# Performance work log

Hardware: AMD Instinct MI355X
Metric: run time of the kernel (lower is better)

Reference implementation:

```python
import itertools
import jax, jax.numpy as jnp
import numpy as np

ALPHA = 1e-4   # mse/conn mixing
BETA = 0.1
DMAX = 20.0
NCAP = 10.0    # costs_n_cap
PCAP = 3.0     # costs_p_cap
W3D = 64       # 3D cube window (window_3d)
W2D = 32       # 2D MALIS window (window_2d, default)


def _dilate5(mask):
    # scipy binary_dilation, default cross structuring element, 5 iterations
    m = mask.astype(bool)
    for _ in range(5):
        p = np.pad(m, 1)
        m = p[1:-1, 1:-1] | p[:-2, 1:-1] | p[2:, 1:-1] | p[1:-1, :-2] | p[1:-1, 2:]
    return m


def _label8(mask):
    # skimage.measure.label on boolean mask: 8-connectivity, background=0
    H, W = mask.shape
    lbl = np.zeros((H, W), np.int64)
    parent = {}

    def find(x):
        while parent[x] != x:
            parent[x] = parent[parent[x]]
            x = parent[x]
        return x

    nxt = 1
    for i in range(H):
        for j in range(W):
            if not mask[i, j]:
                continue
            neigh = []
            for di, dj in ((-1, -1), (-1, 0), (-1, 1), (0, -1)):
                ii, jj = i + di, j + dj
                if 0 <= ii < H and 0 <= jj < W and mask[ii, jj]:
                    neigh.append(int(lbl[ii, jj]))
            if not neigh:
                lbl[i, j] = nxt
                parent[nxt] = nxt
                nxt += 1
            else:
                m0 = min(neigh)
                lbl[i, j] = m0
                for nb in neigh:
                    ra, rb = find(m0), find(nb)
                    if ra != rb:
                        parent[max(ra, rb)] = min(ra, rb)
    out = np.zeros_like(lbl)
    remap = {}
    c = 0
    for i in range(H):
        for j in range(W):
            if lbl[i, j] > 0:
                r = find(int(lbl[i, j]))
                if r not in remap:
                    c += 1
                    remap[r] = c
                out[i, j] = remap[r]
    return out


def _malis_edge_weights(seg, n1, n2, costs, pos):
    # MALIS union-find / Kruskal maximal-spanning-tree pair counting.
    # Edges processed in descending cost order. Background (seg==0) nodes
    # are not counted. pos=1: #same-label pairs merged; pos=0: #diff-label pairs.
    n = seg.size
    parent = list(range(n))

    def find(x):
        r = x
        while parent[r] != r:
            r = parent[r]
        while parent[x] != r:
            parent[x], x = r, parent[x]
        return r

    cnt = [({int(s): 1} if s > 0 else {}) for s in seg]
    tot = [1 if s > 0 else 0 for s in seg]
    w = np.zeros(costs.shape[0], np.float32)
    for e in np.argsort(-costs, kind="stable"):
        ra, rb = find(int(n1[e])), find(int(n2[e]))
        if ra == rb:
            continue
        ca, cb = cnt[ra], cnt[rb]
        if len(ca) > len(cb):
            ra, rb, ca, cb = rb, ra, cb, ca
        same = 0
        for l, v in ca.items():
            same += v * cb.get(l, 0)
        w[e] = float(same if pos else tot[ra] * tot[rb] - same)
        for l, v in ca.items():
            cb[l] = cb.get(l, 0) + v
        tot[rb] += tot[ra]
        parent[ra] = rb
        cnt[ra] = None
    return w


def _window_weights(pred2d, tgt2d):
    # numpy MALIS node weights for a [B,1,H,W] 2D projection
    B, C, H, W = pred2d.shape
    w = W2D
    wn = np.zeros(pred2d.shape, np.float32)
    wp = np.zeros(pred2d.shape, np.float32)
    idx = np.arange(w * w).reshape(w, w)
    n1 = np.concatenate([idx[:, :-1].ravel(), idx[:-1, :].ravel()])
    n2 = np.concatenate([idx[:, 1:].ravel(), idx[1:, :].ravel()])
    nh = w * (w - 1)
    for k in range(H // w):
        for j in range(W // w):
            p = pred2d[:, :, k*w:(k+1)*w, j*w:(j+1)*w]
            t = tgt2d[:, :, k*w:(k+1)*w, j*w:(j+1)*w]
            ch = (p[:, :, :, :-1] + p[:, :, :, 1:]).reshape(B, -1)
            cv = (p[:, :, :-1, :] + p[:, :, 1:, :]).reshape(B, -1)
            costs = np.concatenate([ch, cv], 1).astype(np.float32)
            gh = (t[:, :, :, :-1] + t[:, :, :, 1:]).reshape(B, -1)
            gv = (t[:, :, :-1, :] + t[:, :, 1:, :]).reshape(B, -1)
            gt = np.concatenate([gh, gv], 1).astype(np.float32)
            costs_n = costs.copy()
            costs_p = costs.copy()
            costs_n[gt > NCAP] = NCAP
            costs_p[gt < PCAP] = 0.0
            gt = np.minimum(gt, NCAP)
            for b in range(B):
                sg = _label8(~_dilate5(t[b, 0] == 0)).ravel()
                en = _malis_edge_weights(sg, n1, n2, costs_n[b], 0)
                ep = _malis_edge_weights(sg, n1, n2, costs_p[b], 1)
                sn = en.sum()
                if sn > 0:
                    en = en / sn
                sp = ep.sum()
                if sp > 0:
                    ep = ep / sp
                en[gt[b] >= PCAP] = 0.0
                ep[gt[b] < NCAP] = 0.0
                for ew, out in ((en, wn), (ep, wp)):
                    eh = ew[:nh].reshape(w, w - 1)
                    ev = ew[nh:].reshape(w - 1, w)
                    nwt = np.zeros((w, w), np.float32)
                    nwt[:, :-1] += eh
                    nwt[:, 1:] += eh
                    nwt[:-1, :] += ev
                    nwt[1:, :] += ev
                    out[b, 0, k*w:(k+1)*w, j*w:(j+1)*w] = nwt
    return wn, wp


def _precompute(pred_np, tgt_np):
    # host-side (detached) MALIS weight maps, exactly as the torch module
    B, C, H, W, D = pred_np.shape
    items = []
    for k, j, i in itertools.product(range(H // W3D), range(W // W3D), range(D // W3D)):
        sl = (slice(None), slice(None), slice(k*W3D, (k+1)*W3D),
              slice(j*W3D, (j+1)*W3D), slice(i*W3D, (i+1)*W3D))
        pc, tc = pred_np[sl], tgt_np[sl]
        for axis in (2, 3, 4):
            wn, wp = _window_weights(pc.min(axis=axis), tc.min(axis=axis))
            items.append((k, j, i, axis, jnp.asarray(wn), jnp.asarray(wp)))
    return items


def _loss(pred, target, items):
    mse = jnp.mean((pred - target) ** 2)
    conn = jnp.float32(0.0)
    for (k, j, i, axis, wn, wp) in items:
        pc = pred[:, :, k*W3D:(k+1)*W3D, j*W3D:(j+1)*W3D, i*W3D:(i+1)*W3D]
        proj = jnp.min(pc, axis=axis)  # [B,1,64,64]
        conn = conn + jnp.sum(proj**2 * wn + BETA * (DMAX - proj)**2 * wp)
    return (mse, jnp.float32(ALPHA) * conn)


def setup_inputs() -> dict:
    # synthetic distance-transform-like volumes (zeros on 'vessel' seeds)
    rng = np.random.default_rng(0)
    B, H = 4, 128
    g = np.arange(H, dtype=np.float32)
    zz, yy, xx = np.meshgrid(g, g, g, indexing="ij")
    tgt = np.empty((B, 1, H, H, H), np.float32)
    for b in range(B):
        pts = rng.uniform(0, H, size=(24, 3)).astype(np.float32)
        d = np.full((H, H, H), np.inf, np.float32)
        for p in pts:
            d = np.minimum(d, np.sqrt((zz - p[0])**2 + (yy - p[1])**2 + (xx - p[2])**2))
        tgt[b, 0] = np.floor(np.minimum(d, DMAX))
    pred = np.clip(tgt + 0.5 * rng.standard_normal(tgt.shape).astype(np.float32), 0.0, DMAX).astype(np.float32)
    return {"pred": jnp.asarray(pred), "target": jnp.asarray(tgt)}


def reference(pred, target):
    items = _precompute(np.asarray(pred), np.asarray(target))
    return _loss(pred, target, items)
```

## Files before the change

kernel.cpp:

```cpp
#include <hip/hip_runtime.h>

#define BLOCK 256
#define NNODE 1024
#define NH    992
#define NE    1984
#define NSORT 2048
#define LMAX  12
#define CHUNK 64
#define NPASS (NE / CHUNK)

typedef unsigned long long ull;

__device__ __forceinline__ void edge_nodes(int e, int& a, int& b) {
    if (e < NH) {
        int r = e / 31;
        int c = e - r * 31;
        a = (r << 5) + c;
        b = a + 1;
    } else {
        a = e - NH;
        b = a + 32;
    }
}

__device__ __forceinline__ int find_par(unsigned short* par, int x) {
    volatile unsigned short* vp = par;
    int r = x;
    int p = vp[r];
    while (p != r) { r = p; p = vp[r]; }
    int c = x;
    while (c != r) { const int nxt = vp[c]; vp[c] = (unsigned short)r; c = nxt; }
    return r;
}

__device__ __forceinline__ int dot16x4(ull a, ull b) {
    int s  = (int)(a & 0xFFFFu)         * (int)(b & 0xFFFFu);
    s     += (int)((a >> 16) & 0xFFFFu) * (int)((b >> 16) & 0xFFFFu);
    s     += (int)((a >> 32) & 0xFFFFu) * (int)((b >> 32) & 0xFFFFu);
    s     += (int)((a >> 48) & 0xFFFFu) * (int)((b >> 48) & 0xFFFFu);
    return s;
}

__device__ __forceinline__ void cswap(unsigned int& ka, unsigned short& ia,
                                      unsigned int& kb, unsigned short& ib, bool up) {
    const bool gt = (ka > kb) || (ka == kb && ia > ib);
    if (gt == up) {
        const unsigned int  tk = ka; ka = kb; kb = tk;
        const unsigned short ti = ia; ia = ib; ib = ti;
    }
}

template<int MODE>
__device__ __forceinline__ void kruskal_run(unsigned short* sh_parent,
                                            unsigned int*   sh_szto,
                                            ull*            sh_cnt64,
                                            unsigned int*   sh_key,
                                            const unsigned short* sh_idx,
                                            const int sign, const int lane) {
    unsigned int* claim32 = (unsigned int*)sh_cnt64;
    for (int pass = 0; pass < NPASS; ++pass) {
        const int e = sh_idx[pass * CHUNK + lane];
        int a, bb; edge_nodes(e, a, bb);
        int ra = find_par(sh_parent, a);
        int rb = find_par(sh_parent, bb);
        bool cand = (ra != rb);

        if (MODE < 3) {
            for (int round = 0; round < 3; ++round) {
                const unsigned int tag =
                    ((unsigned int)(pass * 4 + round + 1) << 6) | (unsigned int)(63 - lane);
                const int ia = ra * 6 + 2 * MODE;
                const int ib = rb * 6 + 2 * MODE;
                if (cand) {
                    atomicMax(&claim32[ia], tag);
                    atomicMax(&claim32[ib], tag);
                }
                asm volatile("s_waitcnt lgkmcnt(0)" ::: "memory");
                __builtin_amdgcn_sched_barrier(0);
                bool win = false;
                if (cand) win = (claim32[ia] == tag) && (claim32[ib] == tag);
                if (win) {
                    const unsigned int xa = sh_szto[ra], xb = sh_szto[rb];
                    const int ta = (int)(xa >> 16), tb = (int)(xb >> 16);
                    int wv;
                    ull a0 = 0, a1 = 0, b0 = 0, b1 = 0;
                    if (MODE == 0) {
                        wv = ta * tb;
                    } else {
                        a0 = sh_cnt64[ra * 3]; b0 = sh_cnt64[rb * 3];
                        int same = dot16x4(a0, b0);
                        if (MODE >= 2) {
                            a1 = sh_cnt64[ra * 3 + 1]; b1 = sh_cnt64[rb * 3 + 1];
                            same += dot16x4(a1, b1);
                        }
                        wv = sign ? same : (ta * tb - same);
                    }
                    const int big = ((xa & 0xFFFFu) > (xb & 0xFFFFu));
                    const int rs = big ? ra : rb;
                    const int rl = big ? rb : ra;
                    sh_key[e] = __float_as_uint((float)wv);
                    sh_szto[rs] = xa + xb;
                    if (MODE >= 1 && (ta + tb) > 0) {
                        sh_cnt64[rs * 3] = a0 + b0;
                        if (MODE >= 2) sh_cnt64[rs * 3 + 1] = a1 + b1;
                    }
                    sh_parent[rl] = (unsigned short)rs;
                    cand = false;
                }
                asm volatile("s_waitcnt lgkmcnt(0)" ::: "memory");
                __builtin_amdgcn_sched_barrier(0);
                if (cand) {
                    ra = find_par(sh_parent, ra);
                    rb = find_par(sh_parent, rb);
                    cand = (ra != rb);
                }
                const ull P = __ballot(cand);
                if (__popcll(P) < 10) break;
            }
        }

        ull m = __ballot(cand);
        while (m) {
            const int i = (int)__builtin_ctzll(m);
            m &= m - 1;
            const unsigned int pack = (unsigned int)ra | ((unsigned int)rb << 10) | ((unsigned int)e << 20);
            const unsigned int pk = (unsigned int)__shfl((int)pack, i);
            const int ra_i = (int)(pk & 1023u);
            const int rb_i = (int)((pk >> 10) & 1023u);
            if (ra_i == rb_i) continue;
            const int se = (int)(pk >> 20);
            const unsigned int xa = sh_szto[ra_i], xb = sh_szto[rb_i];
            const int ta = (int)(xa >> 16), tb = (int)(xb >> 16);
            const int big = ((xa & 0xFFFFu) > (xb & 0xFFFFu));
            const int rs = big ? ra_i : rb_i;
            const int rl = big ? rb_i : ra_i;
            int wv;
            if (MODE == 0) {
                wv = ta * tb;
            } else {
                const ull a0 = sh_cnt64[ra_i * 3 + 0];
                const ull b0 = sh_cnt64[rb_i * 3 + 0];
                ull a1 = 0, a2 = 0, b1 = 0, b2 = 0;
                int same = dot16x4(a0, b0);
                if (MODE >= 2) {
                    a1 = sh_cnt64[ra_i * 3 + 1]; b1 = sh_cnt64[rb_i * 3 + 1];
                    same += dot16x4(a1, b1);
                }
                if (MODE >= 3) {
                    a2 = sh_cnt64[ra_i * 3 + 2]; b2 = sh_cnt64[rb_i * 3 + 2];
                    same += dot16x4(a2, b2);
                }
                wv = sign ? same : (ta * tb - same);
                if (lane == 0 && (ta + tb) > 0) {
                    sh_cnt64[rs * 3 + 0] = a0 + b0;
                    if (MODE >= 2) sh_cnt64[rs * 3 + 1] = a1 + b1;
                    if (MODE >= 3) sh_cnt64[rs * 3 + 2] = a2 + b2;
                }
            }
            if (lane == 0) {
                sh_key[se] = __float_as_uint((float)wv);
                sh_szto[rs] = xa + xb;
                sh_parent[rl] = (unsigned short)rs;
            }
            if (ra == rl) ra = rs;
            if (rb == rl) rb = rs;
        }
    }
}

template<int MODE>
__device__ __forceinline__ void uf_init(unsigned short* sh_parent,
                                        unsigned int* sh_szto,
                                        ull* sh_cnt64,
                                        const unsigned char* sh_seg,
                                        const int tid) {
    for (int pix = tid; pix < NNODE; pix += BLOCK) {
        sh_parent[pix] = (unsigned short)pix;
        const int s = sh_seg[pix];
        const unsigned int tot = (s > 0 && s <= LMAX) ? 1u : 0u;
        sh_szto[pix] = 1u | (tot << 16);
        ull c0 = 0, c1 = 0, c2 = 0;
        if (s >= 1 && s <= LMAX) {
            const ull bit = 1ull << (((s - 1) & 3) * 16);
            const int q = (s - 1) >> 2;
            if (q == 0) c0 = bit; else if (q == 1) c1 = bit; else c2 = bit;
        }
        if (MODE == 0) {
            sh_cnt64[pix * 3 + 0] = 0ull;
        } else if (MODE == 1) {
            sh_cnt64[pix * 3 + 0] = c0;
            sh_cnt64[pix * 3 + 1] = 0ull;
        } else if (MODE == 2) {
            sh_cnt64[pix * 3 + 0] = c0;
            sh_cnt64[pix * 3 + 1] = c1;
            sh_cnt64[pix * 3 + 2] = 0ull;
        } else {
            sh_cnt64[pix * 3 + 0] = c0;
            sh_cnt64[pix * 3 + 1] = c1;
            sh_cnt64[pix * 3 + 2] = c2;
        }
    }
}

__global__ __launch_bounds__(BLOCK) void prep_kernel(const float* __restrict__ pred,
                                                     const float* __restrict__ tgt,
                                                     char* __restrict__ ws,
                                                     double* __restrict__ acc_ws,
                                                     int B) {
    __shared__ alignas(16) float sh_p[NNODE];
    __shared__ alignas(16) float sh_t[NNODE];
    __shared__ unsigned char  mA[NNODE];
    __shared__ unsigned char  mB[NNODE];
    __shared__ unsigned short sh_parent[NNODE];
    __shared__ unsigned short sh_lab[NNODE];
    __shared__ int sh_flag;
    __shared__ int sh_L;
    __shared__ double sh_redp[4];

    const int tid = threadIdx.x;
    const int w = blockIdx.x;
    int wg = w;
    const int b    = wg % B;  wg /= B;
    const int win  = wg & 3;  wg >>= 2;
    const int item = wg;
    const int axis_id = item % 3;
    const int cube = item / 3;
    const int ci = cube & 1;
    const int cj = (cube >> 1) & 1;
    const int ck = (cube >> 2) & 1;
    const int wk = win >> 1;
    const int wj = win & 1;

    const int NW = 96 * B;
    float* Pb = (float*)(ws + 64);
    float* Tb = Pb + (size_t)NW * NNODE;
    unsigned char* Sb = (unsigned char*)(Tb + (size_t)NW * NNODE);
    int* Lb = (int*)(Sb + (size_t)NW * NNODE);

    const size_t base = (size_t)b * 2097152u;

    if (axis_id == 2) {
        double msum = 0.0;
        for (int pix = tid; pix < NNODE; pix += BLOCK) {
            const int r = pix >> 5, c = pix & 31;
            const int R = wk * 32 + r, C = wj * 32 + c;
            const size_t idx0 = base + (size_t)(ck * 64 + R) * 16384u + (size_t)(cj * 64 + C) * 128u + (size_t)(ci * 64);
            const float4* pp = reinterpret_cast<const float4*>(pred + idx0);
            const float4* tp = reinterpret_cast<const float4*>(tgt + idx0);
            float pm = 3.4e38f, tm = 3.4e38f;
            #pragma unroll
            for (int h = 0; h < 16; ++h) {
                const float4 a = pp[h];
                const float4 t = tp[h];
                pm = fminf(pm, fminf(fminf(a.x, a.y), fminf(a.z, a.w)));
                tm = fminf(tm, fminf(fminf(t.x, t.y), fminf(t.z, t.w)));
                const float dx = a.x - t.x, dy = a.y - t.y;
                const float dz = a.z - t.z, dw = a.w - t.w;
                msum += (double)(dx * dx);
                msum += (double)(dy * dy);
                msum += (double)(dz * dz);
                msum += (double)(dw * dw);
            }
            sh_p[pix] = pm;
            sh_t[pix] = tm;
        }
        for (int off = 32; off > 0; off >>= 1) msum += __shfl_down(msum, off, 64);
        if ((tid & 63) == 0) sh_redp[tid >> 6] = msum;
        __syncthreads();
        if (tid == 0)
            atomicAdd(&acc_ws[0], sh_redp[0] + sh_redp[1] + sh_redp[2] + sh_redp[3]);
    } else {
        const int r  = tid >> 3;
        const int c0 = (tid & 7) << 2;
        const int R = wk * 32 + r, C = wj * 32 + c0;
        size_t idx0; int hstride;
        if (axis_id == 0) {
            idx0 = base + (size_t)(ck * 64) * 16384u + (size_t)(cj * 64 + R) * 128u + (size_t)(ci * 64 + C);
            hstride = 16384;
        } else {
            idx0 = base + (size_t)(ck * 64 + R) * 16384u + (size_t)(cj * 64) * 128u + (size_t)(ci * 64 + C);
            hstride = 128;
        }
        float4 pm = make_float4(3.4e38f, 3.4e38f, 3.4e38f, 3.4e38f);
        float4 tm = pm;
        #pragma unroll 8
        for (int h = 0; h < 64; ++h) {
            const float4 a  = *reinterpret_cast<const float4*>(pred + idx0);
            const float4 t4 = *reinterpret_cast<const float4*>(tgt + idx0);
            pm.x = fminf(pm.x, a.x);  pm.y = fminf(pm.y, a.y);
            pm.z = fminf(pm.z, a.z);  pm.w = fminf(pm.w, a.w);
            tm.x = fminf(tm.x, t4.x); tm.y = fminf(tm.y, t4.y);
            tm.z = fminf(tm.z, t4.z); tm.w = fminf(tm.w, t4.w);
            idx0 += (size_t)hstride;
        }
        *reinterpret_cast<float4*>(&sh_p[(r << 5) + c0]) = pm;
        *reinterpret_cast<float4*>(&sh_t[(r << 5) + c0]) = tm;
        __syncthreads();
    }

    for (int pix = tid; pix < NNODE; pix += BLOCK)
        mA[pix] = (sh_t[pix] == 0.0f) ? 1 : 0;
    __syncthreads();
    for (int it = 0; it < 5; ++it) {
        unsigned char* src = (it & 1) ? mB : mA;
        unsigned char* dst = (it & 1) ? mA : mB;
        for (int pix = tid; pix < NNODE; pix += BLOCK) {
            const int r = pix >> 5, c = pix & 31;
            unsigned char v = src[pix];
            if (r > 0)  v |= src[pix - 32];
            if (r < 31) v |= src[pix + 32];
            if (c > 0)  v |= src[pix - 1];
            if (c < 31) v |= src[pix + 1];
            dst[pix] = v;
        }
        __syncthreads();
    }
    for (int pix = tid; pix < NNODE; pix += BLOCK)
        mA[pix] = mB[pix] ^ 1;
    __syncthreads();

    for (int pix = tid; pix < NNODE; pix += BLOCK)
        sh_parent[pix] = mA[pix] ? (unsigned short)pix : (unsigned short)0xFFFF;
    __syncthreads();
    for (;;) {
        if (tid == 0) sh_flag = 0;
        __syncthreads();
        for (int pix = tid; pix < NNODE; pix += BLOCK) {
            if (!mA[pix]) continue;
            const int r = pix >> 5, c = pix & 31;
            int m = sh_parent[pix];
            #pragma unroll
            for (int d = 0; d < 8; ++d) {
                static const int dr[8] = {-1,-1,-1, 0, 0, 1, 1, 1};
                static const int dc[8] = {-1, 0, 1,-1, 1,-1, 0, 1};
                const int rr = r + dr[d], cc = c + dc[d];
                if (rr < 0 || rr > 31 || cc < 0 || cc > 31) continue;
                const int nb = (rr << 5) + cc;
                if (mA[nb]) { int v = sh_parent[nb]; if (v < m) m = v; }
            }
            while ((int)sh_parent[m] < m) m = sh_parent[m];
            if (m < (int)sh_parent[pix]) { sh_parent[pix] = (unsigned short)m; sh_flag = 1; }
        }
        __syncthreads();
        const int f = sh_flag;
        __syncthreads();
        if (f == 0) break;
    }

    if (tid == 0) sh_L = 0;
    __syncthreads();
    for (int pix = tid; pix < NNODE; pix += BLOCK) {
        if (mA[pix] && (int)sh_parent[pix] == pix) {
            const int id = atomicAdd(&sh_L, 1);
            sh_lab[pix] = (unsigned short)(id + 1);
        }
    }
    __syncthreads();

    {
        const int p4 = tid << 2;
        *reinterpret_cast<float4*>(&Pb[(size_t)w * NNODE + p4]) =
            *reinterpret_cast<const float4*>(&sh_p[p4]);
        *reinterpret_cast<float4*>(&Tb[(size_t)w * NNODE + p4]) =
            *reinterpret_cast<const float4*>(&sh_t[p4]);
        unsigned int packed = 0;
        #pragma unroll
        for (int q = 0; q < 4; ++q) {
            const int pix = p4 + q;
            unsigned int s = 0;
            if (mA[pix]) {
                int lab = sh_lab[sh_parent[pix]];
                if (lab > 255) lab = 255;
                s = (unsigned int)lab;
            }
            packed |= s << (q * 8);
        }
        ((unsigned int*)Sb)[(size_t)w * (NNODE / 4) + tid] = packed;
        if (tid == 0) Lb[w] = sh_L;
    }
}

__global__ __launch_bounds__(BLOCK) void solve_kernel(const char* __restrict__ ws_c,
                                                      double* __restrict__ acc_ws,
                                                      int B) {
    __shared__ alignas(16) float          sh_p[NNODE];
    __shared__ alignas(16) float          sh_t[NNODE];
    __shared__ alignas(16) unsigned int   sh_key[NSORT];
    __shared__ alignas(16) unsigned short sh_idx[NSORT];
    __shared__ unsigned short sh_parent[NNODE];
    __shared__ unsigned int   sh_szto[NNODE];
    __shared__ ull            sh_cnt64[NNODE * 3];
    __shared__ alignas(16) unsigned char sh_seg[NNODE];
    __shared__ float          sh_sn;
    __shared__ double         sh_red[4];

    const int tid = threadIdx.x;
    int wg = blockIdx.x;
    const int sign = wg & 1;  wg >>= 1;
    const int w = wg;

    const int NW = 96 * B;
    const float* Pb = (const float*)(ws_c + 64);
    const float* Tb = Pb + (size_t)NW * NNODE;
    const unsigned char* Sb = (const unsigned char*)(Tb + (size_t)NW * NNODE);
    const int* Lb = (const int*)(Sb + (size_t)NW * NNODE);

    const int Lraw = Lb[w];
    if (Lraw == 0 || (Lraw == 1 && sign == 0)) return;
    const int mode = (Lraw <= 1) ? 0 : ((Lraw <= 4) ? 1 : ((Lraw <= 8) ? 2 : 3));

    {
        const int p4 = tid << 2;
        *reinterpret_cast<float4*>(&sh_p[p4]) =
            *reinterpret_cast<const float4*>(&Pb[(size_t)w * NNODE + p4]);
        *reinterpret_cast<float4*>(&sh_t[p4]) =
            *reinterpret_cast<const float4*>(&Tb[(size_t)w * NNODE + p4]);
        ((unsigned int*)sh_seg)[tid] =
            ((const unsigned int*)Sb)[(size_t)w * (NNODE / 4) + tid];
    }
    __syncthreads();

    if (mode == 0)      uf_init<0>(sh_parent, sh_szto, sh_cnt64, sh_seg, tid);
    else if (mode == 1) uf_init<1>(sh_parent, sh_szto, sh_cnt64, sh_seg, tid);
    else if (mode == 2) uf_init<2>(sh_parent, sh_szto, sh_cnt64, sh_seg, tid);
    else                uf_init<3>(sh_parent, sh_szto, sh_cnt64, sh_seg, tid);
    __syncthreads();

    unsigned int   K[8];
    unsigned short I[8];
    const int b8 = tid << 3;
    #pragma unroll
    for (int l = 0; l < 8; ++l) {
        const int e = b8 + l;
        if (e < NE) {
            int a, bb; edge_nodes(e, a, bb);
            float cost = sh_p[a] + sh_p[bb];
            const float g = sh_t[a] + sh_t[bb];
            if (sign == 0) { if (g > 10.0f) cost = 10.0f; }
            else           { if (g <  3.0f) cost = 0.0f;  }
            K[l] = ~__float_as_uint(cost);
            I[l] = (unsigned short)e;
        } else {
            K[l] = 0xFFFFFFFFu;
            I[l] = (unsigned short)0xFFFF;
        }
    }
    cswap(K[0],I[0],K[1],I[1], true );
    cswap(K[2],I[2],K[3],I[3], false);
    cswap(K[4],I[4],K[5],I[5], true );
    cswap(K[6],I[6],K[7],I[7], false);
    cswap(K[0],I[0],K[2],I[2], true );
    cswap(K[1],I[1],K[3],I[3], true );
    cswap(K[4],I[4],K[6],I[6], false);
    cswap(K[5],I[5],K[7],I[7], false);
    cswap(K[0],I[0],K[1],I[1], true );
    cswap(K[2],I[2],K[3],I[3], true );
    cswap(K[4],I[4],K[5],I[5], false);
    cswap(K[6],I[6],K[7],I[7], false);
    {
        const bool u8 = ((b8 & 8) == 0);
        cswap(K[0],I[0],K[4],I[4], u8); cswap(K[1],I[1],K[5],I[5], u8);
        cswap(K[2],I[2],K[6],I[6], u8); cswap(K[3],I[3],K[7],I[7], u8);
        cswap(K[0],I[0],K[2],I[2], u8); cswap(K[1],I[1],K[3],I[3], u8);
        cswap(K[4],I[4],K[6],I[6], u8); cswap(K[5],I[5],K[7],I[7], u8);
        cswap(K[0],I[0],K[1],I[1], u8); cswap(K[2],I[2],K[3],I[3], u8);
        cswap(K[4],I[4],K[5],I[5], u8); cswap(K[6],I[6],K[7],I[7], u8);
    }
    {
        uint4 k0, k1, iv;
        k0.x=K[0]; k0.y=K[1]; k0.z=K[2]; k0.w=K[3];
        k1.x=K[4]; k1.y=K[5]; k1.z=K[6]; k1.w=K[7];
        iv.x=(unsigned int)I[0] | ((unsigned int)I[1]<<16);
        iv.y=(unsigned int)I[2] | ((unsigned int)I[3]<<16);
        iv.z=(unsigned int)I[4] | ((unsigned int)I[5]<<16);
        iv.w=(unsigned int)I[6] | ((unsigned int)I[7]<<16);
        *reinterpret_cast<uint4*>(&sh_key[b8])     = k0;
        *reinterpret_cast<uint4*>(&sh_key[b8 + 4]) = k1;
        *reinterpret_cast<uint4*>(&sh_idx[b8])     = iv;
    }
    __syncthreads();

    for (int k = 16; k <= NSORT; k <<= 1) {
        for (int j = k >> 1; j >= 8; j >>= 1) {
            for (int p = tid; p < (NSORT >> 1); p += BLOCK) {
                const int i   = ((p & ~(j - 1)) << 1) | (p & (j - 1));
                const int ixj = i | j;
                const unsigned int ka = sh_key[i], kb = sh_key[ixj];
                const unsigned short ia = sh_idx[i], ib = sh_idx[ixj];
                const bool gt = (ka > kb) || (ka == kb && ia > ib);
                const bool up = ((i & k) == 0);
                if (gt == up) {
                    sh_key[i] = kb; sh_key[ixj] = ka;
                    sh_idx[i] = ib; sh_idx[ixj] = ia;
                }
            }
            __syncthreads();
        }
        {
            const uint4 k0 = *reinterpret_cast<const uint4*>(&sh_key[b8]);
            const uint4 k1 = *reinterpret_cast<const uint4*>(&sh_key[b8 + 4]);
            const uint4 iv = *reinterpret_cast<const uint4*>(&sh_idx[b8]);
            K[0]=k0.x; K[1]=k0.y; K[2]=k0.z; K[3]=k0.w;
            K[4]=k1.x; K[5]=k1.y; K[6]=k1.z; K[7]=k1.w;
            I[0]=(unsigned short)(iv.x); I[1]=(unsigned short)(iv.x>>16);
            I[2]=(unsigned short)(iv.y); I[3]=(unsigned short)(iv.y>>16);
            I[4]=(unsigned short)(iv.z); I[5]=(unsigned short)(iv.z>>16);
            I[6]=(unsigned short)(iv.w); I[7]=(unsigned short)(iv.w>>16);
            const bool u8 = ((b8 & k) == 0);
            cswap(K[0],I[0],K[4],I[4], u8); cswap(K[1],I[1],K[5],I[5], u8);
            cswap(K[2],I[2],K[6],I[6], u8); cswap(K[3],I[3],K[7],I[7], u8);
            cswap(K[0],I[0],K[2],I[2], u8); cswap(K[1],I[1],K[3],I[3], u8);
            cswap(K[4],I[4],K[6],I[6], u8); cswap(K[5],I[5],K[7],I[7], u8);
            cswap(K[0],I[0],K[1],I[1], u8); cswap(K[2],I[2],K[3],I[3], u8);
            cswap(K[4],I[4],K[5],I[5], u8); cswap(K[6],I[6],K[7],I[7], u8);
            uint4 o0, o1, ov;
            o0.x=K[0]; o0.y=K[1]; o0.z=K[2]; o0.w=K[3];
            o1.x=K[4]; o1.y=K[5]; o1.z=K[6]; o1.w=K[7];
            ov.x=(unsigned int)I[0] | ((unsigned int)I[1]<<16);
            ov.y=(unsigned int)I[2] | ((unsigned int)I[3]<<16);
            ov.z=(unsigned int)I[4] | ((unsigned int)I[5]<<16);
            ov.w=(unsigned int)I[6] | ((unsigned int)I[7]<<16);
            *reinterpret_cast<uint4*>(&sh_key[b8])     = o0;
            *reinterpret_cast<uint4*>(&sh_key[b8 + 4]) = o1;
            *reinterpret_cast<uint4*>(&sh_idx[b8])     = ov;
        }
        __syncthreads();
    }

    for (int e = tid; e < NE; e += BLOCK) sh_key[e] = 0u;
    __syncthreads();

    if (tid < 64) {
        if (mode == 0)      kruskal_run<0>(sh_parent, sh_szto, sh_cnt64, sh_key, sh_idx, sign, tid);
        else if (mode == 1) kruskal_run<1>(sh_parent, sh_szto, sh_cnt64, sh_key, sh_idx, sign, tid);
        else if (mode == 2) kruskal_run<2>(sh_parent, sh_szto, sh_cnt64, sh_key, sh_idx, sign, tid);
        else                kruskal_run<3>(sh_parent, sh_szto, sh_cnt64, sh_key, sh_idx, sign, tid);
    }
    __syncthreads();

    {
        float part = 0.0f;
        for (int e = tid; e < NE; e += BLOCK) part += __uint_as_float(sh_key[e]);
        for (int off = 32; off > 0; off >>= 1) part += __shfl_down(part, off, 64);
        if ((tid & 63) == 0) sh_red[tid >> 6] = (double)part;
        __syncthreads();
        if (tid == 0) sh_sn = (float)(sh_red[0] + sh_red[1] + sh_red[2] + sh_red[3]);
        __syncthreads();
    }
    const float sn = sh_sn;

    double acc = 0.0;
    for (int pix = tid; pix < NNODE; pix += BLOCK) {
        const int r = pix >> 5, c = pix & 31;
        float nw = 0.0f;
        if (c < 31) { const int e = r * 31 + c;
            float v = __uint_as_float(sh_key[e]); if (sn > 0.0f) v = v / sn;
            const float g = sh_t[pix] + sh_t[pix + 1];
            if (sign == 0) { if (g >= 3.0f) v = 0.0f; } else { if (g < 10.0f) v = 0.0f; }
            nw += v; }
        if (c > 0)  { const int e = r * 31 + c - 1;
            float v = __uint_as_float(sh_key[e]); if (sn > 0.0f) v = v / sn;
            const float g = sh_t[pix - 1] + sh_t[pix];
            if (sign == 0) { if (g >= 3.0f) v = 0.0f; } else { if (g < 10.0f) v = 0.0f; }
            nw += v; }
        if (r < 31) { const int e = NH + pix;
            float v = __uint_as_float(sh_key[e]); if (sn > 0.0f) v = v / sn;
            const float g = sh_t[pix] + sh_t[pix + 32];
            if (sign == 0) { if (g >= 3.0f) v = 0.0f; } else { if (g < 10.0f) v = 0.0f; }
            nw += v; }
        if (r > 0)  { const int e = NH + pix - 32;
            float v = __uint_as_float(sh_key[e]); if (sn > 0.0f) v = v / sn;
            const float g = sh_t[pix - 32] + sh_t[pix];
            if (sign == 0) { if (g >= 3.0f) v = 0.0f; } else { if (g < 10.0f) v = 0.0f; }
            nw += v; }
        const float p = sh_p[pix];
        float term;
        if (sign == 0) term = (p * p) * nw;
        else { const float d = 20.0f - p; term = (0.1f * (d * d)) * nw; }
        acc += (double)term;
    }
    for (int off = 32; off > 0; off >>= 1) acc += __shfl_down(acc, off, 64);
    if ((tid & 63) == 0) sh_red[tid >> 6] = acc;
    __syncthreads();
    if (tid == 0)
        atomicAdd(&acc_ws[1], sh_red[0] + sh_red[1] + sh_red[2] + sh_red[3]);
}

__global__ __launch_bounds__(BLOCK) void conn_kernel(const float* __restrict__ pred,
                                                     const float* __restrict__ tgt,
                                                     double* __restrict__ acc_ws,
                                                     int B) {
    __shared__ alignas(16) float          sh_p[NNODE];
    __shared__ alignas(16) float          sh_t[NNODE];
    __shared__ alignas(16) unsigned int   sh_key[NSORT];
    __shared__ alignas(16) unsigned short sh_idx[NSORT];
    __shared__ unsigned short sh_parent[NNODE];
    __shared__ unsigned int   sh_szto[NNODE];
    __shared__ ull            sh_cnt64[NNODE * 3];
    __shared__ unsigned char  sh_seg[NNODE];
    __shared__ int            sh_flag;
    __shared__ int            sh_L;
    __shared__ float          sh_sn;
    __shared__ double         sh_red[4];

    const int tid = threadIdx.x;
    int wg = blockIdx.x;
    const int sign = (wg >> 3) & 1;
    wg = (wg & 7) | ((wg >> 4) << 3);
    const int b    = wg % B;  wg /= B;
    const int win  = wg & 3;  wg >>= 2;
    const int item = wg;
    const int axis_id = item % 3;
    const int cube = item / 3;
    const int ci = cube & 1;
    const int cj = (cube >> 1) & 1;
    const int ck = (cube >> 2) & 1;
    const int wk = win >> 1;
    const int wj = win & 1;

    const size_t base = (size_t)b * 2097152u;

    if (axis_id == 2) {
        for (int pix = tid; pix < NNODE; pix += BLOCK) {
            const int r = pix >> 5, c = pix & 31;
            const int R = wk * 32 + r, C = wj * 32 + c;
            const size_t idx0 = base + (size_t)(ck * 64 + R) * 16384u + (size_t)(cj * 64 + C) * 128u + (size_t)(ci * 64);
            const float4* pp = reinterpret_cast<const float4*>(pred + idx0);
            const float4* tp = reinterpret_cast<const float4*>(tgt + idx0);
            float pm = 3.4e38f, tm = 3.4e38f;
            #pragma unroll
            for (int h = 0; h < 16; ++h) {
                const float4 a = pp[h];
                const float4 t = tp[h];
                pm = fminf(pm, fminf(fminf(a.x, a.y), fminf(a.z, a.w)));
                tm = fminf(tm, fminf(fminf(t.x, t.y), fminf(t.z, t.w)));
            }
            sh_p[pix] = pm;
            sh_t[pix] = tm;
        }
    } else {
        const int r  = tid >> 3;
        const int c0 = (tid & 7) << 2;
        const int R = wk * 32 + r, C = wj * 32 + c0;
        size_t idx0; int hstride;
        if (axis_id == 0) {
            idx0 = base + (size_t)(ck * 64) * 16384u + (size_t)(cj * 64 + R) * 128u + (size_t)(ci * 64 + C);
            hstride = 16384;
        } else {
            idx0 = base + (size_t)(ck * 64 + R) * 16384u + (size_t)(cj * 64) * 128u + (size_t)(ci * 64 + C);
            hstride = 128;
        }
        float4 pm = make_float4(3.4e38f, 3.4e38f, 3.4e38f, 3.4e38f);
        float4 tm = pm;
        #pragma unroll 8
        for (int h = 0; h < 64; ++h) {
            const float4 a  = *reinterpret_cast<const float4*>(pred + idx0);
            const float4 t4 = *reinterpret_cast<const float4*>(tgt + idx0);
            pm.x = fminf(pm.x, a.x);  pm.y = fminf(pm.y, a.y);
            pm.z = fminf(pm.z, a.z);  pm.w = fminf(pm.w, a.w);
            tm.x = fminf(tm.x, t4.x); tm.y = fminf(tm.y, t4.y);
            tm.z = fminf(tm.z, t4.z); tm.w = fminf(tm.w, t4.w);
            idx0 += (size_t)hstride;
        }
        *reinterpret_cast<float4*>(&sh_p[(r << 5) + c0]) = pm;
        *reinterpret_cast<float4*>(&sh_t[(r << 5) + c0]) = tm;
    }
    __syncthreads();

    unsigned char* mA = sh_seg;
    unsigned char* mB = (unsigned char*)sh_idx;
    for (int pix = tid; pix < NNODE; pix += BLOCK)
        mA[pix] = (sh_t[pix] == 0.0f) ? 1 : 0;
    __syncthreads();
    for (int it = 0; it < 5; ++it) {
        unsigned char* src = (it & 1) ? mB : mA;
        unsigned char* dst = (it & 1) ? mA : mB;
        for (int pix = tid; pix < NNODE; pix += BLOCK) {
            const int r = pix >> 5, c = pix & 31;
            unsigned char v = src[pix];
            if (r > 0)  v |= src[pix - 32];
            if (r < 31) v |= src[pix + 32];
            if (c > 0)  v |= src[pix - 1];
            if (c < 31) v |= src[pix + 1];
            dst[pix] = v;
        }
        __syncthreads();
    }
    for (int pix = tid; pix < NNODE; pix += BLOCK)
        mA[pix] = mB[pix] ^ 1;
    __syncthreads();

    for (int pix = tid; pix < NNODE; pix += BLOCK)
        sh_parent[pix] = mA[pix] ? (unsigned short)pix : (unsigned short)0xFFFF;
    __syncthreads();
    for (;;) {
        if (tid == 0) sh_flag = 0;
        __syncthreads();
        for (int pix = tid; pix < NNODE; pix += BLOCK) {
            if (!mA[pix]) continue;
            const int r = pix >> 5, c = pix & 31;
            int m = sh_parent[pix];
            #pragma unroll
            for (int d = 0; d < 8; ++d) {
                static const int dr[8] = {-1,-1,-1, 0, 0, 1, 1, 1};
                static const int dc[8] = {-1, 0, 1,-1, 1,-1, 0, 1};
                const int rr = r + dr[d], cc = c + dc[d];
                if (rr < 0 || rr > 31 || cc < 0 || cc > 31) continue;
                const int nb = (rr << 5) + cc;
                if (mA[nb]) { int v = sh_parent[nb]; if (v < m) m = v; }
            }
            while ((int)sh_parent[m] < m) m = sh_parent[m];
            if (m < (int)sh_parent[pix]) { sh_parent[pix] = (unsigned short)m; sh_flag = 1; }
        }
        __syncthreads();
        const int f = sh_flag;
        __syncthreads();
        if (f == 0) break;
    }

    if (tid == 0) sh_L = 0;
    __syncthreads();
    for (int pix = tid; pix < NNODE; pix += BLOCK) {
        if (mA[pix] && (int)sh_parent[pix] == pix) {
            const int id = atomicAdd(&sh_L, 1);
            sh_szto[pix] = (unsigned int)(id + 1);
        }
    }
    __syncthreads();
    for (int pix = tid; pix < NNODE; pix += BLOCK) {
        unsigned char s = 0;
        if (mA[pix]) {
            int lab = (int)sh_szto[sh_parent[pix]];
            if (lab > 255) lab = 255;
            s = (unsigned char)lab;
        }
        sh_seg[pix] = s;
    }
    __syncthreads();

    const int Lraw = sh_L;
    const int mode = (Lraw <= 1) ? 0 : ((Lraw <= 4) ? 1 : ((Lraw <= 8) ? 2 : 3));
    const bool skip_all = (Lraw == 0) || (Lraw == 1 && sign == 0);

    if (!skip_all) {

    if (mode == 0)      uf_init<0>(sh_parent, sh_szto, sh_cnt64, sh_seg, tid);
    else if (mode == 1) uf_init<1>(sh_parent, sh_szto, sh_cnt64, sh_seg, tid);
    else if (mode == 2) uf_init<2>(sh_parent, sh_szto, sh_cnt64, sh_seg, tid);
    else                uf_init<3>(sh_parent, sh_szto, sh_cnt64, sh_seg, tid);
    __syncthreads();

    unsigned int   K[8];
    unsigned short I[8];
    const int b8 = tid << 3;
    #pragma unroll
    for (int l = 0; l < 8; ++l) {
        const int e = b8 + l;
        if (e < NE) {
            int a, bb; edge_nodes(e, a, bb);
            float cost = sh_p[a] + sh_p[bb];
            const float g = sh_t[a] + sh_t[bb];
            if (sign == 0) { if (g > 10.0f) cost = 10.0f; }
            else           { if (g <  3.0f) cost = 0.0f;  }
            K[l] = ~__float_as_uint(cost);
            I[l] = (unsigned short)e;
        } else {
            K[l] = 0xFFFFFFFFu;
            I[l] = (unsigned short)0xFFFF;
        }
    }
    cswap(K[0],I[0],K[1],I[1], true );
    cswap(K[2],I[2],K[3],I[3], false);
    cswap(K[4],I[4],K[5],I[5], true );
    cswap(K[6],I[6],K[7],I[7], false);
    cswap(K[0],I[0],K[2],I[2], true );
    cswap(K[1],I[1],K[3],I[3], true );
    cswap(K[4],I[4],K[6],I[6], false);
    cswap(K[5],I[5],K[7],I[7], false);
    cswap(K[0],I[0],K[1],I[1], true );
    cswap(K[2],I[2],K[3],I[3], true );
    cswap(K[4],I[4],K[5],I[5], false);
    cswap(K[6],I[6],K[7],I[7], false);
    {
        const bool u8 = ((b8 & 8) == 0);
        cswap(K[0],I[0],K[4],I[4], u8); cswap(K[1],I[1],K[5],I[5], u8);
        cswap(K[2],I[2],K[6],I[6], u8); cswap(K[3],I[3],K[7],I[7], u8);
        cswap(K[0],I[0],K[2],I[2], u8); cswap(K[1],I[1],K[3],I[3], u8);
        cswap(K[4],I[4],K[6],I[6], u8); cswap(K[5],I[5],K[7],I[7], u8);
        cswap(K[0],I[0],K[1],I[1], u8); cswap(K[2],I[2],K[3],I[3], u8);
        cswap(K[4],I[4],K[5],I[5], u8); cswap(K[6],I[6],K[7],I[7], u8);
    }
    {
        uint4 k0, k1, iv;
        k0.x=K[0]; k0.y=K[1]; k0.z=K[2]; k0.w=K[3];
        k1.x=K[4]; k1.y=K[5]; k1.z=K[6]; k1.w=K[7];
        iv.x=(unsigned int)I[0] | ((unsigned int)I[1]<<16);
        iv.y=(unsigned int)I[2] | ((unsigned int)I[3]<<16);
        iv.z=(unsigned int)I[4] | ((unsigned int)I[5]<<16);
        iv.w=(unsigned int)I[6] | ((unsigned int)I[7]<<16);
        *reinterpret_cast<uint4*>(&sh_key[b8])     = k0;
        *reinterpret_cast<uint4*>(&sh_key[b8 + 4]) = k1;
        *reinterpret_cast<uint4*>(&sh_idx[b8])     = iv;
    }
    __syncthreads();

    for (int k = 16; k <= NSORT; k <<= 1) {
        for (int j = k >> 1; j >= 8; j >>= 1) {
            for (int p = tid; p < (NSORT >> 1); p += BLOCK) {
                const int i   = ((p & ~(j - 1)) << 1) | (p & (j - 1));
                const int ixj = i | j;
                const unsigned int ka = sh_key[i], kb = sh_key[ixj];
                const unsigned short ia = sh_idx[i], ib = sh_idx[ixj];
                const bool gt = (ka > kb) || (ka == kb && ia > ib);
                const bool up = ((i & k) == 0);
                if (gt == up) {
                    sh_key[i] = kb; sh_key[ixj] = ka;
                    sh_idx[i] = ib; sh_idx[ixj] = ia;
                }
            }
            __syncthreads();
        }
        {
            const uint4 k0 = *reinterpret_cast<const uint4*>(&sh_key[b8]);
            const uint4 k1 = *reinterpret_cast<const uint4*>(&sh_key[b8 + 4]);
            const uint4 iv = *reinterpret_cast<const uint4*>(&sh_idx[b8]);
            K[0]=k0.x; K[1]=k0.y; K[2]=k0.z; K[3]=k0.w;
            K[4]=k1.x; K[5]=k1.y; K[6]=k1.z; K[7]=k1.w;
            I[0]=(unsigned short)(iv.x); I[1]=(unsigned short)(iv.x>>16);
            I[2]=(unsigned short)(iv.y); I[3]=(unsigned short)(iv.y>>16);
            I[4]=(unsigned short)(iv.z); I[5]=(unsigned short)(iv.z>>16);
            I[6]=(unsigned short)(iv.w); I[7]=(unsigned short)(iv.w>>16);
            const bool u8 = ((b8 & k) == 0);
            cswap(K[0],I[0],K[4],I[4], u8); cswap(K[1],I[1],K[5],I[5], u8);
            cswap(K[2],I[2],K[6],I[6], u8); cswap(K[3],I[3],K[7],I[7], u8);
            cswap(K[0],I[0],K[2],I[2], u8); cswap(K[1],I[1],K[3],I[3], u8);
            cswap(K[4],I[4],K[6],I[6], u8); cswap(K[5],I[5],K[7],I[7], u8);
            cswap(K[0],I[0],K[1],I[1], u8); cswap(K[2],I[2],K[3],I[3], u8);
            cswap(K[4],I[4],K[5],I[5], u8); cswap(K[6],I[6],K[7],I[7], u8);
            uint4 o0, o1, ov;
            o0.x=K[0]; o0.y=K[1]; o0.z=K[2]; o0.w=K[3];
            o1.x=K[4]; o1.y=K[5]; o1.z=K[6]; o1.w=K[7];
            ov.x=(unsigned int)I[0] | ((unsigned int)I[1]<<16);
            ov.y=(unsigned int)I[2] | ((unsigned int)I[3]<<16);
            ov.z=(unsigned int)I[4] | ((unsigned int)I[5]<<16);
            ov.w=(unsigned int)I[6] | ((unsigned int)I[7]<<16);
            *reinterpret_cast<uint4*>(&sh_key[b8])     = o0;
            *reinterpret_cast<uint4*>(&sh_key[b8 + 4]) = o1;
            *reinterpret_cast<uint4*>(&sh_idx[b8])     = ov;
        }
        __syncthreads();
    }

    for (int e = tid; e < NE; e += BLOCK) sh_key[e] = 0u;
    __syncthreads();

    if (tid < 64) {
        if (mode == 0)      kruskal_run<0>(sh_parent, sh_szto, sh_cnt64, sh_key, sh_idx, sign, tid);
        else if (mode == 1) kruskal_run<1>(sh_parent, sh_szto, sh_cnt64, sh_key, sh_idx, sign, tid);
        else if (mode == 2) kruskal_run<2>(sh_parent, sh_szto, sh_cnt64, sh_key, sh_idx, sign, tid);
        else                kruskal_run<3>(sh_parent, sh_szto, sh_cnt64, sh_key, sh_idx, sign, tid);
    }
    __syncthreads();

    {
        float part = 0.0f;
        for (int e = tid; e < NE; e += BLOCK) part += __uint_as_float(sh_key[e]);
        for (int off = 32; off > 0; off >>= 1) part += __shfl_down(part, off, 64);
        if ((tid & 63) == 0) sh_red[tid >> 6] = (double)part;
        __syncthreads();
        if (tid == 0) sh_sn = (float)(sh_red[0] + sh_red[1] + sh_red[2] + sh_red[3]);
        __syncthreads();
    }
    const float sn = sh_sn;

    double acc = 0.0;
    for (int pix = tid; pix < NNODE; pix += BLOCK) {
        const int r = pix >> 5, c = pix & 31;
        float nw = 0.0f;
        if (c < 31) { const int e = r * 31 + c;
            float v = __uint_as_float(sh_key[e]); if (sn > 0.0f) v = v / sn;
            const float g = sh_t[pix] + sh_t[pix + 1];
            if (sign == 0) { if (g >= 3.0f) v = 0.0f; } else { if (g < 10.0f) v = 0.0f; }
            nw += v; }
        if (c > 0)  { const int e = r * 31 + c - 1;
            float v = __uint_as_float(sh_key[e]); if (sn > 0.0f) v = v / sn;
            const float g = sh_t[pix - 1] + sh_t[pix];
            if (sign == 0) { if (g >= 3.0f) v = 0.0f; } else { if (g < 10.0f) v = 0.0f; }
            nw += v; }
        if (r < 31) { const int e = NH + pix;
            float v = __uint_as_float(sh_key[e]); if (sn > 0.0f) v = v / sn;
            const float g = sh_t[pix] + sh_t[pix + 32];
            if (sign == 0) { if (g >= 3.0f) v = 0.0f; } else { if (g < 10.0f) v = 0.0f; }
            nw += v; }
        if (r > 0)  { const int e = NH + pix - 32;
            float v = __uint_as_float(sh_key[e]); if (sn > 0.0f) v = v / sn;
            const float g = sh_t[pix - 32] + sh_t[pix];
            if (sign == 0) { if (g >= 3.0f) v = 0.0f; } else { if (g < 10.0f) v = 0.0f; }
            nw += v; }
        const float p = sh_p[pix];
        float term;
        if (sign == 0) term = (p * p) * nw;
        else { const float d = 20.0f - p; term = (0.1f * (d * d)) * nw; }
        acc += (double)term;
    }
    for (int off = 32; off > 0; off >>= 1) acc += __shfl_down(acc, off, 64);
    if ((tid & 63) == 0) sh_red[tid >> 6] = acc;
    __syncthreads();
    if (tid == 0)
        atomicAdd(&acc_ws[1], sh_red[0] + sh_red[1] + sh_red[2] + sh_red[3]);

    }
}

__global__ __launch_bounds__(BLOCK) void mse_kernel(const float* __restrict__ pred,
                                                    const float* __restrict__ tgt,
                                                    double* __restrict__ acc_ws,
                                                    long n) {
    double acc = 0.0;
    for (long i = (long)blockIdx.x * BLOCK + threadIdx.x; i < n; i += (long)gridDim.x * BLOCK) {
        const float d = pred[i] - tgt[i];
        acc += (double)(d * d);
    }
    for (int off = 32; off > 0; off >>= 1) acc += __shfl_down(acc, off, 64);
    __shared__ double red[4];
    if ((threadIdx.x & 63) == 0) red[threadIdx.x >> 6] = acc;
    __syncthreads();
    if (threadIdx.x == 0)
        atomicAdd(&acc_ws[0], red[0] + red[1] + red[2] + red[3]);
}

__global__ void fin_kernel(const double* __restrict__ acc_ws, float* __restrict__ out, long n) {
    if (threadIdx.x == 0 && blockIdx.x == 0) {
        out[0] = (float)(acc_ws[0] / (double)n);
        out[1] = (float)(acc_ws[1] * (double)1e-4f);
    }
}

extern "C" void kernel_launch(void* const* d_in, const int* in_sizes, int n_in,
                              void* d_out, int out_size, void* d_ws, size_t ws_size,
                              hipStream_t stream) {
    const float* pred = (const float*)d_in[0];
    const float* tgt  = (const float*)d_in[1];
    float* out = (float*)d_out;
    double* acc = (double*)d_ws;

    const long n = (long)in_sizes[0];
    const int  B = (int)(n / 2097152);
    const int  NW = 96 * B;
    const size_t need = 64 + (size_t)NW * NNODE * 9 + (size_t)NW * 4;

    hipMemsetAsync(d_ws, 0, 2 * sizeof(double), stream);
    if (ws_size >= need) {
        prep_kernel<<<NW, BLOCK, 0, stream>>>(pred, tgt, (char*)d_ws, acc, B);
        solve_kernel<<<192 * B, BLOCK, 0, stream>>>((const char*)d_ws, acc, B);
    } else {
        mse_kernel<<<1024, BLOCK, 0, stream>>>(pred, tgt, acc, n);
        conn_kernel<<<192 * B, BLOCK, 0, stream>>>(pred, tgt, acc, B);
    }
    fin_kernel<<<1, 64, 0, stream>>>(acc, out, n);
}
```

Baseline: 483.8 us.

## Replace multi-round claim merging with single round plus star-merge prefix scan

Swaps the up-to-three rounds of atomic-claim parallel union for a single claim round. It then adds a fast path for when every remaining candidate edge touches one common giant root G. In that case each small root is deduplicated with atomicMin, and the contributions (sizes and label counts) are combined with a wavefront inclusive prefix scan. This lets every surviving edge get its Kruskal weight in order and be attached to G in one step, cutting the serial ballot loop. It adds shuffle-scan overhead and the fast path only fires when the star pattern holds. It also drops the (ta+tb)>0 guard on the count update and the sequential-order logic is subtle.

```diff
diff --git a/kernel.cpp b/kernel.cpp
--- a/kernel.cpp
+++ b/kernel.cpp
@@ -39,6 +39,12 @@
     s     += (int)((a >> 32) & 0xFFFFu) * (int)((b >> 32) & 0xFFFFu);
     s     += (int)((a >> 48) & 0xFFFFu) * (int)((b >> 48) & 0xFFFFu);
     return s;
+}
+
+__device__ __forceinline__ ull shfl64_up(ull v, int off) {
+    const int lo = __shfl_up((int)(unsigned int)(v & 0xFFFFFFFFu), off, 64);
+    const int hi = __shfl_up((int)(unsigned int)(v >> 32), off, 64);
+    return ((ull)(unsigned int)hi << 32) | (ull)(unsigned int)lo;
 }
 
 __device__ __forceinline__ void cswap(unsigned int& ka, unsigned short& ia,
@@ -66,56 +72,119 @@
         bool cand = (ra != rb);
 
         if (MODE < 3) {
-            for (int round = 0; round < 3; ++round) {
-                const unsigned int tag =
-                    ((unsigned int)(pass * 4 + round + 1) << 6) | (unsigned int)(63 - lane);
-                const int ia = ra * 6 + 2 * MODE;
-                const int ib = rb * 6 + 2 * MODE;
-                if (cand) {
-                    atomicMax(&claim32[ia], tag);
-                    atomicMax(&claim32[ib], tag);
+            const unsigned int tag = ((unsigned int)(pass + 1) << 6) | (unsigned int)(63 - lane);
+            const int ia = ra * 6 + 2 * MODE;
+            const int ib = rb * 6 + 2 * MODE;
+            if (cand) {
+                atomicMax(&claim32[ia], tag);
+                atomicMax(&claim32[ib], tag);
+            }
+            asm volatile("s_waitcnt lgkmcnt(0)" ::: "memory");
+            __builtin_amdgcn_sched_barrier(0);
+            bool win = false;
+            if (cand) win = (claim32[ia] == tag) && (claim32[ib] == tag);
+            if (win) {
+                const unsigned int xa = sh_szto[ra], xb = sh_szto[rb];
+                const int ta = (int)(xa >> 16), tb = (int)(xb >> 16);
+                int wv;
+                ull a0 = 0, a1 = 0, b0 = 0, b1 = 0;
+                if (MODE == 0) {
+                    wv = ta * tb;
+                } else {
+                    a0 = sh_cnt64[ra * 3]; b0 = sh_cnt64[rb * 3];
+                    int same = dot16x4(a0, b0);
+                    if (MODE >= 2) {
+                        a1 = sh_cnt64[ra * 3 + 1]; b1 = sh_cnt64[rb * 3 + 1];
+                        same += dot16x4(a1, b1);
+                    }
+                    wv = sign ? same : (ta * tb - same);
                 }
-                asm volatile("s_waitcnt lgkmcnt(0)" ::: "memory");
-                __builtin_amdgcn_sched_barrier(0);
-                bool win = false;
-                if (cand) win = (claim32[ia] == tag) && (claim32[ib] == tag);
-                if (win) {
-                    const unsigned int xa = sh_szto[ra], xb = sh_szto[rb];
-                    const int ta = (int)(xa >> 16), tb = (int)(xb >> 16);
-                    int wv;
-                    ull a0 = 0, a1 = 0, b0 = 0, b1 = 0;
-                    if (MODE == 0) {
-                        wv = ta * tb;
-                    } else {
-                        a0 = sh_cnt64[ra * 3]; b0 = sh_cnt64[rb * 3];
-                        int same = dot16x4(a0, b0);
-                        if (MODE >= 2) {
-                            a1 = sh_cnt64[ra * 3 + 1]; b1 = sh_cnt64[rb * 3 + 1];
-                            same += dot16x4(a1, b1);
+                const int big = ((xa & 0xFFFFu) > (xb & 0xFFFFu));
+                const int rs = big ? ra : rb;
+                const int rl = big ? rb : ra;
+                sh_key[e] = __float_as_uint((float)wv);
+                sh_szto[rs] = xa + xb;
+                if (MODE >= 1) {
+                    sh_cnt64[rs * 3] = a0 + b0;
+                    if (MODE >= 2) sh_cnt64[rs * 3 + 1] = a1 + b1;
+                }
+                sh_parent[rl] = (unsigned short)rs;
+                cand = false;
+            }
+            asm volatile("s_waitcnt lgkmcnt(0)" ::: "memory");
+            __builtin_amdgcn_sched_barrier(0);
+            if (cand) {
+                ra = find_par(sh_parent, ra);
+                rb = find_par(sh_parent, rb);
+                cand = (ra != rb);
+            }
+
+            const ull P = __ballot(cand);
+            if (__popcll(P) >= 6) {
+                unsigned int xra = 0, xrb = 0;
+                if (cand) { xra = sh_szto[ra]; xrb = sh_szto[rb]; }
+                const int f = (int)__builtin_ctzll(P);
+                const int gc = ((xra & 0xFFFFu) >= (xrb & 0xFFFFu)) ? ra : rb;
+                const int G = __shfl(gc, f);
+                const bool hasG = cand && (ra == G || rb == G);
+                const ull bad = __ballot(cand && !hasG);
+                if (bad == 0ull) {
+                    const int sm = (ra == G) ? rb : ra;
+                    const unsigned int xsm = (ra == G) ? xrb : xra;
+                    if (cand) atomicMin(&claim32[sm * 6 + 2 * MODE], (unsigned int)lane);
+                    asm volatile("s_waitcnt lgkmcnt(0)" ::: "memory");
+                    __builtin_amdgcn_sched_barrier(0);
+                    bool surv = false;
+                    if (cand) surv = (claim32[sm * 6 + 2 * MODE] == (unsigned int)lane);
+                    const unsigned int xG = sh_szto[G];
+                    ull g0 = 0, g1 = 0;
+                    if (MODE >= 1) g0 = sh_cnt64[G * 3];
+                    if (MODE >= 2) g1 = sh_cnt64[G * 3 + 1];
+                    ull c0 = 0, c1 = 0;
+                    if (MODE >= 1 && surv) c0 = sh_cnt64[sm * 3];
+                    if (MODE >= 2 && surv) c1 = sh_cnt64[sm * 3 + 1];
+                    unsigned int sx = surv ? xsm : 0u;
+                    ull s0 = surv ? c0 : 0ull;
+                    ull s1 = surv ? c1 : 0ull;
+                    #pragma unroll
+                    for (int off = 1; off < 64; off <<= 1) {
+                        const unsigned int yx = (unsigned int)__shfl_up((int)sx, off, 64);
+                        ull y0 = 0, y1 = 0;
+                        if (MODE >= 1) y0 = shfl64_up(s0, off);
+                        if (MODE >= 2) y1 = shfl64_up(s1, off);
+                        if (lane >= off) {
+                            sx += yx;
+                            if (MODE >= 1) s0 += y0;
+                            if (MODE >= 2) s1 += y1;
                         }
-                        wv = sign ? same : (ta * tb - same);
                     }
-                    const int big = ((xa & 0xFFFFu) > (xb & 0xFFFFu));
-                    const int rs = big ? ra : rb;
-                    const int rl = big ? rb : ra;
-                    sh_key[e] = __float_as_uint((float)wv);
-                    sh_szto[rs] = xa + xb;
-                    if (MODE >= 1 && (ta + tb) > 0) {
-                        sh_cnt64[rs * 3] = a0 + b0;
-                        if (MODE >= 2) sh_cnt64[rs * 3 + 1] = a1 + b1;
+                    if (surv) {
+                        const unsigned int px = sx - xsm;
+                        const int tG = (int)((xG + px) >> 16);
+                        const int ti = (int)(xsm >> 16);
+                        int wv;
+                        if (MODE == 0) {
+                            wv = tG * ti;
+                        } else {
+                            const ull p0 = s0 - c0;
+                            int same = dot16x4(g0 + p0, c0);
+                            if (MODE >= 2) { const ull p1 = s1 - c1; same += dot16x4(g1 + p1, c1); }
+                            wv = sign ? same : (tG * ti - same);
+                        }
+                        sh_key[e] = __float_as_uint((float)wv);
+                        sh_parent[sm] = (unsigned short)G;
                     }
-                    sh_parent[rl] = (unsigned short)rs;
+                    const ull SV = __ballot(surv);
+                    if (SV != 0ull) {
+                        const int last = 63 - (int)__builtin_clzll(SV);
+                        if (lane == last) {
+                            sh_szto[G] = xG + sx;
+                            if (MODE >= 1) sh_cnt64[G * 3] = g0 + s0;
+                            if (MODE >= 2) sh_cnt64[G * 3 + 1] = g1 + s1;
+                        }
+                    }
                     cand = false;
                 }
-                asm volatile("s_waitcnt lgkmcnt(0)" ::: "memory");
-                __builtin_amdgcn_sched_barrier(0);
-                if (cand) {
-                    ra = find_par(sh_parent, ra);
-                    rb = find_par(sh_parent, rb);
-                    cand = (ra != rb);
-                }
-                const ull P = __ballot(cand);
-                if (__popcll(P) < 10) break;
             }
         }
 
```

Result: no change. 477.9 us (-1.2%).
